# Kernel optimization log

Measured on AMD Instinct MI355X. Metric: run time of the kernel, lower is better.

The kernel has to match this reference:

```python
import jax, jax.numpy as jnp
import numpy as np

B, S, DIM, H, DH = 2, 2048, 1024, 16, 64
INNER = H * DH


def setup_inputs() -> dict:
    key = jax.random.key(0)
    ks = jax.random.split(key, 4)
    sd = 0.02
    return {
        "x": jax.random.normal(ks[0], (B, S, DIM), dtype=jnp.float32),
        "ln_w": jnp.ones((DIM,), jnp.float32),
        "ln_b": jnp.zeros((DIM,), jnp.float32),
        "Wq": jax.random.normal(ks[1], (DIM, INNER), jnp.float32) * sd,
        "Wkv": jax.random.normal(ks[2], (DIM, 2 * INNER), jnp.float32) * sd,
        "q_gamma": jnp.ones((H, 1, DH), jnp.float32),
        "k_gamma": jnp.ones((H, 1, DH), jnp.float32),
        "Wo": jax.random.normal(ks[3], (INNER, DIM), jnp.float32) * sd,
    }


def _rmsnorm(t, gamma, scale):
    # t: (b,h,s,d); gamma: (h,1,d)
    normed = t * jax.lax.rsqrt(jnp.mean(t * t, axis=-1, keepdims=True) + 1e-8)
    return normed * scale * gamma


def reference(x, ln_w, ln_b, Wq, Wkv, q_gamma, k_gamma, Wo):
    h, dh = q_gamma.shape[0], q_gamma.shape[-1]
    b, s, _ = x.shape
    # pre-LayerNorm (eps 1e-5, biased variance)
    mean = jnp.mean(x, axis=-1, keepdims=True)
    var = jnp.var(x, axis=-1, keepdims=True)
    xn = ln_w * (x - mean) / jnp.sqrt(var + 1e-5) + ln_b
    # projections
    q = xn @ Wq                       # (b,s,h*dh)
    k, v = jnp.split(xn @ Wkv, 2, axis=-1)
    # split heads -> (b,h,s,dh)
    to_heads = lambda t: t.reshape(b, s, h, dh).transpose(0, 2, 1, 3)
    q, k, v = to_heads(q), to_heads(k), to_heads(v)
    scale = dh ** 0.5
    q = _rmsnorm(q, q_gamma, scale)
    k = _rmsnorm(k, k_gamma, scale)
    # attention (no extra 1/sqrt(d): RMSNorm scale already applied)
    dots = jnp.einsum("bhid,bhjd->bhij", q, k)
    attn = jax.nn.softmax(dots, axis=-1)
    out = jnp.einsum("bhij,bhjd->bhid", attn, v)
    out = out.transpose(0, 2, 1, 3).reshape(b, s, h * dh)
    return out @ Wo
```

## Files before the change

kernel.cpp:

```cpp
#include <hip/hip_runtime.h>
#include <hip/hip_bf16.h>

#define DEVFN __device__ __forceinline__

typedef __attribute__((ext_vector_type(8))) short short8;
typedef __attribute__((ext_vector_type(4))) short short4v;
typedef __attribute__((ext_vector_type(4))) float f32x4;

#define MFMA(a,b,c) __builtin_amdgcn_mfma_f32_16x16x32_bf16((a),(b),(c),0,0,0)

DEVFN void gload_lds16(const __hip_bfloat16* g, __hip_bfloat16* l) {
  __builtin_amdgcn_global_load_lds((const __attribute__((address_space(1))) void*)g,
                                   (__attribute__((address_space(3))) void*)l, 16, 0, 0);
}

DEVFN float bf2f(__hip_bfloat16 h) { return __bfloat162float(h); }
DEVFN __hip_bfloat16 f2bf(float f) { return __float2bfloat16(f); }

DEVFN void store_out(float* p, float v) { *p = v; }
DEVFN void store_out(__hip_bfloat16* p, float v) { *p = f2bf(v); }

__global__ __launch_bounds__(256) void ln_split_kernel(
    const float* __restrict__ x, const float* __restrict__ lw, const float* __restrict__ lb,
    __hip_bfloat16* __restrict__ xh, __hip_bfloat16* __restrict__ xl) {
  int row = blockIdx.x, t = threadIdx.x;
  float4 v = ((const float4*)(x + (size_t)row * 1024))[t];
  float s  = v.x + v.y + v.z + v.w;
  float ss = v.x*v.x + v.y*v.y + v.z*v.z + v.w*v.w;
  #pragma unroll
  for (int m = 1; m < 64; m <<= 1) { s += __shfl_xor(s, m); ss += __shfl_xor(ss, m); }
  __shared__ float red[8];
  int wv = t >> 6;
  if ((t & 63) == 0) { red[wv] = s; red[4 + wv] = ss; }
  __syncthreads();
  s  = red[0] + red[1] + red[2] + red[3];
  ss = red[4] + red[5] + red[6] + red[7];
  float mean = s * (1.f/1024.f);
  float var  = ss * (1.f/1024.f) - mean*mean;
  float inv  = rsqrtf(var + 1e-5f);
  float4 wv4 = ((const float4*)lw)[t];
  float4 bv4 = ((const float4*)lb)[t];
  float xv[4] = {v.x, v.y, v.z, v.w};
  float wa[4] = {wv4.x, wv4.y, wv4.z, wv4.w};
  float ba[4] = {bv4.x, bv4.y, bv4.z, bv4.w};
  union { short4v s4; __hip_bfloat16 h[4]; } uh, ul;
  #pragma unroll
  for (int j = 0; j < 4; ++j) {
    float val = (xv[j] - mean) * inv * wa[j] + ba[j];
    __hip_bfloat16 hi = f2bf(val);
    uh.h[j] = hi;
    ul.h[j] = f2bf(val - bf2f(hi));
  }
  ((short4v*)(xh + (size_t)row * 1024))[t] = uh.s4;
  ((short4v*)(xl + (size_t)row * 1024))[t] = ul.s4;
}

__global__ __launch_bounds__(256) void wprep_kernel(
    const float* __restrict__ Wq, const float* __restrict__ Wkv, const float* __restrict__ Wo,
    __hip_bfloat16* __restrict__ Wqk_h, __hip_bfloat16* __restrict__ Wqk_l,
    __hip_bfloat16* __restrict__ Wv, __hip_bfloat16* __restrict__ Wot) {
  __shared__ float tile[64][68];
  int bid = blockIdx.x, t = threadIdx.x;
  const float* src; int srcN, kt, nt, drow;
  __hip_bfloat16 *dh, *dl;
  if (bid < 256) {
    src = Wq; srcN = 1024; kt = bid >> 4; nt = bid & 15;
    dh = Wqk_h; dl = Wqk_l; drow = nt * 64;
  } else if (bid < 768) {
    int r = bid - 256; src = Wkv; srcN = 2048; kt = r >> 5; nt = r & 31;
    if (nt < 16) { dh = Wqk_h; dl = Wqk_l; drow = 1024 + nt * 64; }
    else         { dh = Wv;    dl = nullptr; drow = (nt - 16) * 64; }
  } else {
    int r = bid - 768; src = Wo; srcN = 1024; kt = r >> 4; nt = r & 15;
    dh = Wot; dl = nullptr; drow = nt * 64;
  }
  int lr = t >> 2, c = t & 3;
  const float* sp = src + (size_t)(kt*64 + lr) * srcN + nt*64 + c*16;
  float* tr = &tile[lr][c*16];
  ((float4*)tr)[0] = ((const float4*)sp)[0];
  ((float4*)tr)[1] = ((const float4*)sp)[1];
  ((float4*)tr)[2] = ((const float4*)sp)[2];
  ((float4*)tr)[3] = ((const float4*)sp)[3];
  __syncthreads();
  union { short8 s8[2]; __hip_bfloat16 h[16]; } hh, ll;
  #pragma unroll
  for (int e = 0; e < 16; ++e) {
    float wv = tile[c*16 + e][lr];
    __hip_bfloat16 hi = f2bf(wv);
    hh.h[e] = hi;
    ll.h[e] = f2bf(wv - bf2f(hi));
  }
  size_t doff = (size_t)(drow + lr) * 1024 + kt*64 + c*16;
  ((short8*)(dh + doff))[0] = hh.s8[0];
  ((short8*)(dh + doff))[1] = hh.s8[1];
  if (dl) {
    ((short8*)(dl + doff))[0] = ll.s8[0];
    ((short8*)(dl + doff))[1] = ll.s8[1];
  }
}

__global__ __launch_bounds__(256) void gemm_dual_kernel(
    const __hip_bfloat16* __restrict__ Ah, const __hip_bfloat16* __restrict__ Al,
    const __hip_bfloat16* __restrict__ Bh, const __hip_bfloat16* __restrict__ Bl,
    __hip_bfloat16* __restrict__ Ch, __hip_bfloat16* __restrict__ Cl,
    const float* __restrict__ qg, const float* __restrict__ kg) {
  __shared__ __align__(16) __hip_bfloat16 sAh[128*32], sAl[128*32], sBh[128*32], sBl[128*32];
  const int K = 1024, N = 2048;
  int mt = blockIdx.x, nt = blockIdx.y;
  int t = threadIdx.x, w = t >> 6, l = t & 63;
  int wr = w >> 1, wc = w & 1, lr = l & 15, lk = (l >> 4) * 8;
  f32x4 acc[4][4] = {};
  for (int k0 = 0; k0 < K; k0 += 32) {
    #pragma unroll
    for (int i = 0; i < 2; ++i) {
      int ci = i*256 + t;
      size_t ga = (size_t)(mt*128 + (ci >> 2)) * K + k0 + (ci & 3) * 8;
      size_t gb = (size_t)(nt*128 + (ci >> 2)) * K + k0 + (ci & 3) * 8;
      int ldst = (i*256 + w*64) * 8;
      gload_lds16(Ah + ga, sAh + ldst);
      gload_lds16(Al + ga, sAl + ldst);
      gload_lds16(Bh + gb, sBh + ldst);
      gload_lds16(Bl + gb, sBl + ldst);
    }
    __syncthreads();
    short8 ah[4], al[4], bh[4], bl[4];
    #pragma unroll
    for (int m = 0; m < 4; ++m) {
      int ro = (wr*64 + m*16 + lr)*32 + lk;
      ah[m] = *(const short8*)(sAh + ro);
      al[m] = *(const short8*)(sAl + ro);
    }
    #pragma unroll
    for (int n = 0; n < 4; ++n) {
      int ro = (wc*64 + n*16 + lr)*32 + lk;
      bh[n] = *(const short8*)(sBh + ro);
      bl[n] = *(const short8*)(sBl + ro);
    }
    #pragma unroll
    for (int m = 0; m < 4; ++m)
      #pragma unroll
      for (int n = 0; n < 4; ++n) {
        acc[m][n] = MFMA(ah[m], bh[n], acc[m][n]);
        acc[m][n] = MFMA(ah[m], bl[n], acc[m][n]);
        acc[m][n] = MFMA(al[m], bh[n], acc[m][n]);
      }
    __syncthreads();
  }
  int col0 = nt*128 + wc*64;
  int head = col0 >> 6;
  const float* gamma = (head < 16) ? (qg + head*64) : (kg + (head - 16)*64);
  float g[4];
  #pragma unroll
  for (int nf = 0; nf < 4; ++nf) g[nf] = gamma[nf*16 + lr];
  #pragma unroll
  for (int m = 0; m < 4; ++m) {
    #pragma unroll
    for (int r = 0; r < 4; ++r) {
      float ss2 = 0.f;
      #pragma unroll
      for (int nf = 0; nf < 4; ++nf) ss2 += acc[m][nf][r] * acc[m][nf][r];
      #pragma unroll
      for (int msk = 1; msk < 16; msk <<= 1) ss2 += __shfl_xor(ss2, msk);
      float scl = rsqrtf(ss2 * (1.f/64.f) + 1e-8f) * 8.f;
      int row = mt*128 + wr*64 + m*16 + (l >> 4)*4 + r;
      #pragma unroll
      for (int nf = 0; nf < 4; ++nf) {
        float val = acc[m][nf][r] * scl * g[nf];
        __hip_bfloat16 hi = f2bf(val);
        size_t off = (size_t)row * N + col0 + nf*16 + lr;
        Ch[off] = hi;
        Cl[off] = f2bf(val - bf2f(hi));
      }
    }
  }
}

template <typename OUT_T>
__global__ __launch_bounds__(256) void gemm_single_kernel(
    const __hip_bfloat16* __restrict__ A, const __hip_bfloat16* __restrict__ Bt,
    OUT_T* __restrict__ C, int N) {
  __shared__ __align__(16) __hip_bfloat16 sA[128*32], sB[128*32];
  const int K = 1024;
  int mt = blockIdx.x, nt = blockIdx.y;
  int t = threadIdx.x, w = t >> 6, l = t & 63;
  int wr = w >> 1, wc = w & 1, lr = l & 15, lk = (l >> 4) * 8;
  f32x4 acc[4][4] = {};
  for (int k0 = 0; k0 < K; k0 += 32) {
    #pragma unroll
    for (int i = 0; i < 2; ++i) {
      int ci = i*256 + t;
      size_t ga = (size_t)(mt*128 + (ci >> 2)) * K + k0 + (ci & 3) * 8;
      size_t gb = (size_t)(nt*128 + (ci >> 2)) * K + k0 + (ci & 3) * 8;
      int ldst = (i*256 + w*64) * 8;
      gload_lds16(A + ga, sA + ldst);
      gload_lds16(Bt + gb, sB + ldst);
    }
    __syncthreads();
    short8 af[4], bf[4];
    #pragma unroll
    for (int m = 0; m < 4; ++m) af[m] = *(const short8*)(sA + (wr*64 + m*16 + lr)*32 + lk);
    #pragma unroll
    for (int n = 0; n < 4; ++n) bf[n] = *(const short8*)(sB + (wc*64 + n*16 + lr)*32 + lk);
    #pragma unroll
    for (int m = 0; m < 4; ++m)
      #pragma unroll
      for (int n = 0; n < 4; ++n)
        acc[m][n] = MFMA(af[m], bf[n], acc[m][n]);
    __syncthreads();
  }
  int row0 = mt*128 + wr*64, col0 = nt*128 + wc*64;
  #pragma unroll
  for (int m = 0; m < 4; ++m)
    #pragma unroll
    for (int n = 0; n < 4; ++n)
      #pragma unroll
      for (int r = 0; r < 4; ++r) {
        int row = row0 + m*16 + (l >> 4)*4 + r;
        int col = col0 + n*16 + lr;
        store_out(&C[(size_t)row * N + col], acc[m][n][r]);
      }
}

__global__ __launch_bounds__(256) void vtrans_kernel(
    const __hip_bfloat16* __restrict__ vbuf, __hip_bfloat16* __restrict__ vT) {
  __shared__ __hip_bfloat16 tile[64][72];
  int bid = blockIdx.x;
  int b = bid >> 9, h = (bid >> 5) & 15, st = bid & 31;
  int t = threadIdx.x, j = t >> 2, c = t & 3;
  const short8* src = (const short8*)(vbuf + (size_t)(b*2048 + st*64 + j) * 1024 + h*64 + c*16);
  *(short8*)&tile[j][c*16]     = src[0];
  *(short8*)&tile[j][c*16 + 8] = src[1];
  __syncthreads();
  int d = t >> 2, c2 = t & 3;
  union { short8 s8[2]; __hip_bfloat16 hh[16]; } o;
  #pragma unroll
  for (int e = 0; e < 16; ++e) o.hh[e] = tile[c2*16 + e][d];
  short8* dst = (short8*)(vT + (size_t)((b*16 + h)*64 + d) * 2048 + st*64 + c2*16);
  dst[0] = o.s8[0];
  dst[1] = o.s8[1];
}

__global__ __launch_bounds__(256) void attn_kernel(
    const __hip_bfloat16* __restrict__ qk_h, const __hip_bfloat16* __restrict__ qk_l,
    const __hip_bfloat16* __restrict__ vT, __hip_bfloat16* __restrict__ ao) {
  __shared__ __align__(16) __hip_bfloat16 sKh[2][4096], sKl[2][4096], sVt[2][4096];
  __shared__ __align__(16) __hip_bfloat16 sP[4096];
  int t = threadIdx.x, w = t >> 6, l = t & 63, lr = l & 15, hi = l >> 4, lk = hi * 8;
  int bh = blockIdx.x & 31, qt = blockIdx.x >> 5;
  int b = bh >> 4, h = bh & 15;
  const __hip_bfloat16* qbh = qk_h + (size_t)b * 2048 * 2048 + h * 64;
  const __hip_bfloat16* qbl = qk_l + (size_t)b * 2048 * 2048 + h * 64;
  const __hip_bfloat16* kbh = qbh + 1024;
  const __hip_bfloat16* kbl = qbl + 1024;
  const __hip_bfloat16* vtb = vT + (size_t)bh * 64 * 2048;
  int qrow = qt*64 + w*16 + lr;
  short8 qh0 = *(const short8*)(qbh + (size_t)qrow*2048 + lk);
  short8 qh1 = *(const short8*)(qbh + (size_t)qrow*2048 + 32 + lk);
  short8 ql0 = *(const short8*)(qbl + (size_t)qrow*2048 + lk);
  short8 ql1 = *(const short8*)(qbl + (size_t)qrow*2048 + 32 + lk);
  f32x4 o_acc[4] = {};
  f32x4 l_acc = {0.f, 0.f, 0.f, 0.f};
  float m_run[4];
  #pragma unroll
  for (int r = 0; r < 4; ++r) m_run[r] = -1e30f;
  const short8 ones = {0x3F80, 0x3F80, 0x3F80, 0x3F80, 0x3F80, 0x3F80, 0x3F80, 0x3F80};

  int swl = lr & 7;
  int c0e = (hi ^ swl) << 3;
  int c1e = c0e ^ 32;
  int ci0 = t, ci1 = 256 + t;
  int r0 = ci0 >> 3, cs0 = (ci0 & 7) ^ (r0 & 7);
  int r1 = ci1 >> 3, cs1 = (ci1 & 7) ^ (r1 & 7);
  int ldb0 = (w*64) * 8, ldb1 = (256 + w*64) * 8;

#define STAGE(B, KV) do { \
    gload_lds16(kbh + (size_t)((KV) + r0)*2048 + cs0*8, &sKh[B][0] + ldb0); \
    gload_lds16(kbh + (size_t)((KV) + r1)*2048 + cs1*8, &sKh[B][0] + ldb1); \
    gload_lds16(kbl + (size_t)((KV) + r0)*2048 + cs0*8, &sKl[B][0] + ldb0); \
    gload_lds16(kbl + (size_t)((KV) + r1)*2048 + cs1*8, &sKl[B][0] + ldb1); \
    gload_lds16(vtb + (size_t)r0*2048 + (KV) + cs0*8, &sVt[B][0] + ldb0); \
    gload_lds16(vtb + (size_t)r1*2048 + (KV) + cs1*8, &sVt[B][0] + ldb1); \
  } while (0)

  STAGE(0, 0);
  int buf = 0;
  for (int tile = 0; tile < 32; ++tile) {
    int kv0 = tile << 6;
    if (tile < 31) {
      STAGE(buf ^ 1, kv0 + 64);
      asm volatile("s_waitcnt vmcnt(6)" ::: "memory");
    } else {
      asm volatile("s_waitcnt vmcnt(0)" ::: "memory");
    }
    __builtin_amdgcn_s_barrier();
    const __hip_bfloat16* pKh = &sKh[buf][0];
    const __hip_bfloat16* pKl = &sKl[buf][0];
    const __hip_bfloat16* pVt = &sVt[buf][0];
    f32x4 s_acc[4];
    __builtin_amdgcn_s_setprio(1);
    #pragma unroll
    for (int nf = 0; nf < 4; ++nf) {
      int rb = (nf*16 + lr) * 64;
      short8 kh0 = *(const short8*)(pKh + rb + c0e);
      short8 kh1 = *(const short8*)(pKh + rb + c1e);
      short8 kl0 = *(const short8*)(pKl + rb + c0e);
      short8 kl1 = *(const short8*)(pKl + rb + c1e);
      f32x4 sa = {};
      sa = MFMA(qh0, kh0, sa);
      sa = MFMA(qh1, kh1, sa);
      sa = MFMA(qh0, kl0, sa);
      sa = MFMA(qh1, kl1, sa);
      sa = MFMA(ql0, kh0, sa);
      sa = MFMA(ql1, kh1, sa);
      s_acc[nf] = sa;
    }
    __builtin_amdgcn_s_setprio(0);
    bool need = false;
    #pragma unroll
    for (int r = 0; r < 4; ++r) {
      float thr = m_run[r] + 8.f;
      #pragma unroll
      for (int nf = 0; nf < 4; ++nf) need |= (s_acc[nf][r] > thr);
    }
    if (__any(need)) {
      #pragma unroll
      for (int r = 0; r < 4; ++r) {
        float mx = fmaxf(fmaxf(s_acc[0][r], s_acc[1][r]), fmaxf(s_acc[2][r], s_acc[3][r]));
        #pragma unroll
        for (int msk = 1; msk < 16; msk <<= 1) mx = fmaxf(mx, __shfl_xor(mx, msk));
        float mnew = fmaxf(m_run[r], mx);
        float corr = __expf(m_run[r] - mnew);
        m_run[r] = mnew;
        l_acc[r] *= corr;
        #pragma unroll
        for (int df = 0; df < 4; ++df) o_acc[df][r] *= corr;
      }
    }
    #pragma unroll
    for (int r = 0; r < 4; ++r) {
      int prow = hi*4 + r;
      int pbase = (w << 10) + prow*64 + swl;
      #pragma unroll
      for (int nf = 0; nf < 4; ++nf) {
        float pv = __expf(s_acc[nf][r] - m_run[r]);
        int chunk = (nf << 1) | (lr >> 3);
        sP[pbase + ((chunk ^ (prow & 7)) << 3)] = f2bf(pv);
      }
    }
    __builtin_amdgcn_s_setprio(1);
    #pragma unroll
    for (int kk = 0; kk < 2; ++kk) {
      int vck = (((kk << 2) | hi) ^ swl) << 3;
      short8 pf = *(const short8*)(sP + (w << 10) + lr*64 + vck);
      l_acc = MFMA(pf, ones, l_acc);
      #pragma unroll
      for (int df = 0; df < 4; ++df) {
        short8 vf = *(const short8*)(pVt + (df*16 + lr)*64 + vck);
        o_acc[df] = MFMA(pf, vf, o_acc[df]);
      }
    }
    __builtin_amdgcn_s_setprio(0);
    __builtin_amdgcn_s_barrier();
    buf ^= 1;
  }
#undef STAGE
  size_t orow0 = (size_t)b*2048 + qt*64 + w*16 + hi*4;
  #pragma unroll
  for (int df = 0; df < 4; ++df)
    #pragma unroll
    for (int r = 0; r < 4; ++r) {
      float oval = o_acc[df][r] / l_acc[r];
      ao[(orow0 + r) * 1024 + h*64 + df*16 + lr] = f2bf(oval);
    }
}

extern "C" void kernel_launch(void* const* d_in, const int* in_sizes, int n_in,
                              void* d_out, int out_size, void* d_ws, size_t ws_size,
                              hipStream_t stream) {
  const float* x   = (const float*)d_in[0];
  const float* lw  = (const float*)d_in[1];
  const float* lb  = (const float*)d_in[2];
  const float* Wq  = (const float*)d_in[3];
  const float* Wkv = (const float*)d_in[4];
  const float* qg  = (const float*)d_in[5];
  const float* kg  = (const float*)d_in[6];
  const float* Wo  = (const float*)d_in[7];
  float* out = (float*)d_out;
  char* ws = (char*)d_ws;
  const size_t MB = 1024 * 1024;
  __hip_bfloat16* xh    = (__hip_bfloat16*)(ws + 0);
  __hip_bfloat16* xl    = (__hip_bfloat16*)(ws + 8*MB);
  __hip_bfloat16* qk_h  = (__hip_bfloat16*)(ws + 16*MB);
  __hip_bfloat16* qk_l  = (__hip_bfloat16*)(ws + 32*MB);
  __hip_bfloat16* Wqk_h = (__hip_bfloat16*)(ws + 48*MB);
  __hip_bfloat16* Wqk_l = (__hip_bfloat16*)(ws + 52*MB);
  __hip_bfloat16* Wv    = (__hip_bfloat16*)(ws + 56*MB);
  __hip_bfloat16* Wot   = (__hip_bfloat16*)(ws + 58*MB);
  __hip_bfloat16* vT    = (__hip_bfloat16*)(ws + 60*MB);
  __hip_bfloat16* vbuf  = (__hip_bfloat16*)(ws + 8*MB);
  __hip_bfloat16* ao    = (__hip_bfloat16*)(ws + 0);

  ln_split_kernel<<<4096, 256, 0, stream>>>(x, lw, lb, xh, xl);
  wprep_kernel<<<1024, 256, 0, stream>>>(Wq, Wkv, Wo, Wqk_h, Wqk_l, Wv, Wot);
  gemm_dual_kernel<<<dim3(32, 16), 256, 0, stream>>>(xh, xl, Wqk_h, Wqk_l, qk_h, qk_l, qg, kg);
  gemm_single_kernel<__hip_bfloat16><<<dim3(32, 8), 256, 0, stream>>>(xh, Wv, vbuf, 1024);
  vtrans_kernel<<<1024, 256, 0, stream>>>(vbuf, vT);
  attn_kernel<<<1024, 256, 0, stream>>>(qk_h, qk_l, vT, ao);
  gemm_single_kernel<float><<<dim3(32, 8), 256, 0, stream>>>(ao, Wot, out, 1024);
}
```

Before: 318.9 us.

## Double-buffer GEMM LDS loads, halve single-GEMM N tile, fold log2e into Q

New measurement: 320.0 us. Within noise of the previous version (+0.4%).

```diff
diff --git a/kernel.cpp b/kernel.cpp
--- a/kernel.cpp
+++ b/kernel.cpp
@@ -8,6 +8,7 @@
 typedef __attribute__((ext_vector_type(4))) float f32x4;
 
 #define MFMA(a,b,c) __builtin_amdgcn_mfma_f32_16x16x32_bf16((a),(b),(c),0,0,0)
+#define LOG2E 1.4426950408889634f
 
 DEVFN void gload_lds16(const __hip_bfloat16* g, __hip_bfloat16* l) {
   __builtin_amdgcn_global_load_lds((const __attribute__((address_space(1))) void*)g,
@@ -104,38 +105,54 @@
     const __hip_bfloat16* __restrict__ Bh, const __hip_bfloat16* __restrict__ Bl,
     __hip_bfloat16* __restrict__ Ch, __hip_bfloat16* __restrict__ Cl,
     const float* __restrict__ qg, const float* __restrict__ kg) {
-  __shared__ __align__(16) __hip_bfloat16 sAh[128*32], sAl[128*32], sBh[128*32], sBl[128*32];
+  __shared__ __align__(16) __hip_bfloat16 sAh[2][4096], sAl[2][4096], sBh[2][4096], sBl[2][4096];
   const int K = 1024, N = 2048;
   int mt = blockIdx.x, nt = blockIdx.y;
   int t = threadIdx.x, w = t >> 6, l = t & 63;
   int wr = w >> 1, wc = w & 1, lr = l & 15, lk = (l >> 4) * 8;
   f32x4 acc[4][4] = {};
+  int r0 = t >> 2, r1 = 64 + (t >> 2), ko = (t & 3) * 8;
+  int ldb0 = (w*64) * 8, ldb1 = (256 + w*64) * 8;
+
+#define GSTAGE(B, K0) do { \
+    gload_lds16(Ah + (size_t)(mt*128 + r0)*K + (K0) + ko, &sAh[B][0] + ldb0); \
+    gload_lds16(Ah + (size_t)(mt*128 + r1)*K + (K0) + ko, &sAh[B][0] + ldb1); \
+    gload_lds16(Al + (size_t)(mt*128 + r0)*K + (K0) + ko, &sAl[B][0] + ldb0); \
+    gload_lds16(Al + (size_t)(mt*128 + r1)*K + (K0) + ko, &sAl[B][0] + ldb1); \
+    gload_lds16(Bh + (size_t)(nt*128 + r0)*K + (K0) + ko, &sBh[B][0] + ldb0); \
+    gload_lds16(Bh + (size_t)(nt*128 + r1)*K + (K0) + ko, &sBh[B][0] + ldb1); \
+    gload_lds16(Bl + (size_t)(nt*128 + r0)*K + (K0) + ko, &sBl[B][0] + ldb0); \
+    gload_lds16(Bl + (size_t)(nt*128 + r1)*K + (K0) + ko, &sBl[B][0] + ldb1); \
+  } while (0)
+
+  GSTAGE(0, 0);
+  int buf = 0;
   for (int k0 = 0; k0 < K; k0 += 32) {
-    #pragma unroll
-    for (int i = 0; i < 2; ++i) {
-      int ci = i*256 + t;
-      size_t ga = (size_t)(mt*128 + (ci >> 2)) * K + k0 + (ci & 3) * 8;
-      size_t gb = (size_t)(nt*128 + (ci >> 2)) * K + k0 + (ci & 3) * 8;
-      int ldst = (i*256 + w*64) * 8;
-      gload_lds16(Ah + ga, sAh + ldst);
-      gload_lds16(Al + ga, sAl + ldst);
-      gload_lds16(Bh + gb, sBh + ldst);
-      gload_lds16(Bl + gb, sBl + ldst);
-    }
-    __syncthreads();
+    if (k0 + 32 < K) {
+      GSTAGE(buf ^ 1, k0 + 32);
+      asm volatile("s_waitcnt vmcnt(8)" ::: "memory");
+    } else {
+      asm volatile("s_waitcnt vmcnt(0)" ::: "memory");
+    }
+    __builtin_amdgcn_s_barrier();
+    const __hip_bfloat16* pAh = &sAh[buf][0];
+    const __hip_bfloat16* pAl = &sAl[buf][0];
+    const __hip_bfloat16* pBh = &sBh[buf][0];
+    const __hip_bfloat16* pBl = &sBl[buf][0];
     short8 ah[4], al[4], bh[4], bl[4];
     #pragma unroll
     for (int m = 0; m < 4; ++m) {
       int ro = (wr*64 + m*16 + lr)*32 + lk;
-      ah[m] = *(const short8*)(sAh + ro);
-      al[m] = *(const short8*)(sAl + ro);
+      ah[m] = *(const short8*)(pAh + ro);
+      al[m] = *(const short8*)(pAl + ro);
     }
     #pragma unroll
     for (int n = 0; n < 4; ++n) {
       int ro = (wc*64 + n*16 + lr)*32 + lk;
-      bh[n] = *(const short8*)(sBh + ro);
-      bl[n] = *(const short8*)(sBl + ro);
-    }
+      bh[n] = *(const short8*)(pBh + ro);
+      bl[n] = *(const short8*)(pBl + ro);
+    }
+    __builtin_amdgcn_s_setprio(1);
     #pragma unroll
     for (int m = 0; m < 4; ++m)
       #pragma unroll
@@ -144,11 +161,15 @@
         acc[m][n] = MFMA(ah[m], bl[n], acc[m][n]);
         acc[m][n] = MFMA(al[m], bh[n], acc[m][n]);
       }
-    __syncthreads();
-  }
+    __builtin_amdgcn_s_setprio(0);
+    __builtin_amdgcn_s_barrier();
+    buf ^= 1;
+  }
+#undef GSTAGE
   int col0 = nt*128 + wc*64;
   int head = col0 >> 6;
   const float* gamma = (head < 16) ? (qg + head*64) : (kg + (head - 16)*64);
+  float qscale = (head < 16) ? LOG2E : 1.0f;
   float g[4];
   #pragma unroll
   for (int nf = 0; nf < 4; ++nf) g[nf] = gamma[nf*16 + lr];
@@ -161,7 +182,7 @@
       for (int nf = 0; nf < 4; ++nf) ss2 += acc[m][nf][r] * acc[m][nf][r];
       #pragma unroll
       for (int msk = 1; msk < 16; msk <<= 1) ss2 += __shfl_xor(ss2, msk);
-      float scl = rsqrtf(ss2 * (1.f/64.f) + 1e-8f) * 8.f;
+      float scl = rsqrtf(ss2 * (1.f/64.f) + 1e-8f) * 8.f * qscale;
       int row = mt*128 + wr*64 + m*16 + (l >> 4)*4 + r;
       #pragma unroll
       for (int nf = 0; nf < 4; ++nf) {
@@ -179,40 +200,54 @@
 __global__ __launch_bounds__(256) void gemm_single_kernel(
     const __hip_bfloat16* __restrict__ A, const __hip_bfloat16* __restrict__ Bt,
     OUT_T* __restrict__ C, int N) {
-  __shared__ __align__(16) __hip_bfloat16 sA[128*32], sB[128*32];
+  __shared__ __align__(16) __hip_bfloat16 sA[2][4096], sB[2][2048];
   const int K = 1024;
   int mt = blockIdx.x, nt = blockIdx.y;
   int t = threadIdx.x, w = t >> 6, l = t & 63;
   int wr = w >> 1, wc = w & 1, lr = l & 15, lk = (l >> 4) * 8;
-  f32x4 acc[4][4] = {};
+  f32x4 acc[4][2] = {};
+  int rA0 = t >> 2, rA1 = 64 + (t >> 2), rB = t >> 2, ko = (t & 3) * 8;
+  int ldb0 = (w*64) * 8, ldb1 = (256 + w*64) * 8;
+
+#define GS(B, K0) do { \
+    gload_lds16(A  + (size_t)(mt*128 + rA0)*K + (K0) + ko, &sA[B][0] + ldb0); \
+    gload_lds16(A  + (size_t)(mt*128 + rA1)*K + (K0) + ko, &sA[B][0] + ldb1); \
+    gload_lds16(Bt + (size_t)(nt*64  + rB )*K + (K0) + ko, &sB[B][0] + ldb0); \
+  } while (0)
+
+  GS(0, 0);
+  int buf = 0;
   for (int k0 = 0; k0 < K; k0 += 32) {
-    #pragma unroll
-    for (int i = 0; i < 2; ++i) {
-      int ci = i*256 + t;
-      size_t ga = (size_t)(mt*128 + (ci >> 2)) * K + k0 + (ci & 3) * 8;
-      size_t gb = (size_t)(nt*128 + (ci >> 2)) * K + k0 + (ci & 3) * 8;
-      int ldst = (i*256 + w*64) * 8;
-      gload_lds16(A + ga, sA + ldst);
-      gload_lds16(Bt + gb, sB + ldst);
-    }
-    __syncthreads();
-    short8 af[4], bf[4];
-    #pragma unroll
-    for (int m = 0; m < 4; ++m) af[m] = *(const short8*)(sA + (wr*64 + m*16 + lr)*32 + lk);
-    #pragma unroll
-    for (int n = 0; n < 4; ++n) bf[n] = *(const short8*)(sB + (wc*64 + n*16 + lr)*32 + lk);
+    if (k0 + 32 < K) {
+      GS(buf ^ 1, k0 + 32);
+      asm volatile("s_waitcnt vmcnt(3)" ::: "memory");
+    } else {
+      asm volatile("s_waitcnt vmcnt(0)" ::: "memory");
+    }
+    __builtin_amdgcn_s_barrier();
+    const __hip_bfloat16* pA = &sA[buf][0];
+    const __hip_bfloat16* pB = &sB[buf][0];
+    short8 af[4], bf[2];
+    #pragma unroll
+    for (int m = 0; m < 4; ++m) af[m] = *(const short8*)(pA + (wr*64 + m*16 + lr)*32 + lk);
+    #pragma unroll
+    for (int n = 0; n < 2; ++n) bf[n] = *(const short8*)(pB + (wc*32 + n*16 + lr)*32 + lk);
+    __builtin_amdgcn_s_setprio(1);
     #pragma unroll
     for (int m = 0; m < 4; ++m)
       #pragma unroll
-      for (int n = 0; n < 4; ++n)
+      for (int n = 0; n < 2; ++n)
         acc[m][n] = MFMA(af[m], bf[n], acc[m][n]);
-    __syncthreads();
-  }
-  int row0 = mt*128 + wr*64, col0 = nt*128 + wc*64;
+    __builtin_amdgcn_s_setprio(0);
+    __builtin_amdgcn_s_barrier();
+    buf ^= 1;
+  }
+#undef GS
+  int row0 = mt*128 + wr*64, col0 = nt*64 + wc*32;
   #pragma unroll
   for (int m = 0; m < 4; ++m)
     #pragma unroll
-    for (int n = 0; n < 4; ++n)
+    for (int n = 0; n < 2; ++n)
       #pragma unroll
       for (int r = 0; r < 4; ++r) {
         int row = row0 + m*16 + (l >> 4)*4 + r;
@@ -264,6 +299,7 @@
   #pragma unroll
   for (int r = 0; r < 4; ++r) m_run[r] = -1e30f;
   const short8 ones = {0x3F80, 0x3F80, 0x3F80, 0x3F80, 0x3F80, 0x3F80, 0x3F80, 0x3F80};
+  const float THR = 8.f * LOG2E;
 
   int swl = lr & 7;
   int c0e = (hi ^ swl) << 3;
@@ -318,7 +354,7 @@
     bool need = false;
     #pragma unroll
     for (int r = 0; r < 4; ++r) {
-      float thr = m_run[r] + 8.f;
+      float thr = m_run[r] + THR;
       #pragma unroll
       for (int nf = 0; nf < 4; ++nf) need |= (s_acc[nf][r] > thr);
     }
@@ -329,7 +365,7 @@
         #pragma unroll
         for (int msk = 1; msk < 16; msk <<= 1) mx = fmaxf(mx, __shfl_xor(mx, msk));
         float mnew = fmaxf(m_run[r], mx);
-        float corr = __expf(m_run[r] - mnew);
+        float corr = exp2f(m_run[r] - mnew);
         m_run[r] = mnew;
         l_acc[r] *= corr;
         #pragma unroll
@@ -342,7 +378,7 @@
       int pbase = (w << 10) + prow*64 + swl;
       #pragma unroll
       for (int nf = 0; nf < 4; ++nf) {
-        float pv = __expf(s_acc[nf][r] - m_run[r]);
+        float pv = exp2f(s_acc[nf][r] - m_run[r]);
         int chunk = (nf << 1) | (lr >> 3);
         sP[pbase + ((chunk ^ (prow & 7)) << 3)] = f2bf(pv);
       }
@@ -403,8 +439,8 @@
   ln_split_kernel<<<4096, 256, 0, stream>>>(x, lw, lb, xh, xl);
   wprep_kernel<<<1024, 256, 0, stream>>>(Wq, Wkv, Wo, Wqk_h, Wqk_l, Wv, Wot);
   gemm_dual_kernel<<<dim3(32, 16), 256, 0, stream>>>(xh, xl, Wqk_h, Wqk_l, qk_h, qk_l, qg, kg);
-  gemm_single_kernel<__hip_bfloat16><<<dim3(32, 8), 256, 0, stream>>>(xh, Wv, vbuf, 1024);
+  gemm_single_kernel<__hip_bfloat16><<<dim3(32, 16), 256, 0, stream>>>(xh, Wv, vbuf, 1024);
   vtrans_kernel<<<1024, 256, 0, stream>>>(vbuf, vT);
   attn_kernel<<<1024, 256, 0, stream>>>(qk_h, qk_l, vT, ao);
-  gemm_single_kernel<float><<<dim3(32, 8), 256, 0, stream>>>(ao, Wot, out, 1024);
-}
+  gemm_single_kernel<float><<<dim3(32, 16), 256, 0, stream>>>(ao, Wot, out, 1024);
+}
```
